# Kernel tuning notes

Hardware: AMD Instinct MI355X
Metric: run time of the kernel (lower is better)

Reference implementation:

```python
import jax, jax.numpy as jnp
import numpy as np

N = 50000      # nodes
E = 1600000    # edges
E_HIDDEN = 256
R_HIDDEN = 128
R = 1000       # number of relations (rel.max()+1)
EPS = 1e-16


def segment_softmax(scores, seg, num_segments):
    # numerically stable softmax over variable-size groups defined by seg
    m = jax.ops.segment_max(scores, seg, num_segments=num_segments)
    ex = jnp.exp(scores - m[seg])
    s = jax.ops.segment_sum(ex, seg, num_segments=num_segments)
    return ex / (s[seg] + EPS)


def setup_inputs() -> dict:
    key = jax.random.key(0)
    ks = jax.random.split(key, 9)
    x_e = jax.random.normal(ks[0], (N, E_HIDDEN), dtype=jnp.float32)
    edge_index = jax.random.randint(ks[1], (2, E), 0, N, dtype=jnp.int64)
    rel = jax.random.randint(ks[2], (E,), 0, R, dtype=jnp.int64)
    # learned params (Linear without bias); stored as [in, out]
    sc_w = 1.0 / np.sqrt(E_HIDDEN)
    sc_a = 1.0 / np.sqrt(R_HIDDEN)
    W_h = jax.random.uniform(ks[3], (E_HIDDEN, R_HIDDEN), jnp.float32, -sc_w, sc_w)
    W_t = jax.random.uniform(ks[4], (E_HIDDEN, R_HIDDEN), jnp.float32, -sc_w, sc_w)
    a_h1 = jax.random.uniform(ks[5], (R_HIDDEN,), jnp.float32, -sc_a, sc_a)
    a_h2 = jax.random.uniform(ks[6], (R_HIDDEN,), jnp.float32, -sc_a, sc_a)
    a_t1 = jax.random.uniform(ks[7], (R_HIDDEN,), jnp.float32, -sc_a, sc_a)
    a_t2 = jax.random.uniform(ks[8], (R_HIDDEN,), jnp.float32, -sc_a, sc_a)
    return {"x_e": x_e, "edge_index": edge_index, "rel": rel,
            "W_h": W_h, "W_t": W_t,
            "a_h1": a_h1, "a_h2": a_h2, "a_t1": a_t1, "a_t2": a_t2}


def reference(x_e, edge_index, rel, W_h, W_t, a_h1, a_h2, a_t1, a_t2):
    h_idx, t_idx = edge_index[0], edge_index[1]
    x_r_h = x_e @ W_h          # [N, r_hidden]
    x_r_t = x_e @ W_t          # [N, r_hidden]
    # per-node scalar scores, gathered per edge
    s_h1 = x_r_h @ a_h1        # [N]
    s_h2 = x_r_t @ a_h2
    s_t1 = x_r_h @ a_t1
    s_t2 = x_r_t @ a_t2
    e1 = s_h1[h_idx] + s_h2[t_idx]   # [E]
    e2 = s_t1[h_idx] + s_t2[t_idx]   # [E]
    alpha1 = segment_softmax(jax.nn.leaky_relu(e1, 0.01), rel, R)
    alpha2 = segment_softmax(jax.nn.leaky_relu(e2, 0.01), rel, R)
    # spmm: out[r] += alpha_e * feat[node_e]
    out_h = jax.ops.segment_sum(alpha1[:, None] * x_r_h[h_idx], rel, num_segments=R)
    out_t = jax.ops.segment_sum(alpha2[:, None] * x_r_t[t_idx], rel, num_segments=R)
    return out_h + out_t       # [R, r_hidden]
```

## Files before the change

### kernel.cpp

```cpp
#include <hip/hip_runtime.h>
#include <hip/hip_fp16.h>
#include <cstdint>
#include <cstddef>

#define E_HID 256
#define R_HID 128
#define NREL  1000
#define EPSF  1e-16f
#define NB    512

__device__ __forceinline__ unsigned encf(float f) {
  unsigned u = __float_as_uint(f);
  return (u & 0x80000000u) ? ~u : (u | 0x80000000u);
}
__device__ __forceinline__ float decf(unsigned u) {
  unsigned b = (u & 0x80000000u) ? (u ^ 0x80000000u) : ~u;
  return __uint_as_float(b);
}

struct h4s { __half2 a, b; };
__device__ __forceinline__ h4s packf4(float4 v) {
  h4s r; r.a = __floats2half2_rn(v.x, v.y); r.b = __floats2half2_rn(v.z, v.w); return r;
}

__global__ __launch_bounds__(256) void k1_gemm(
    const float* __restrict__ xe,
    const float* __restrict__ Wh, const float* __restrict__ Wt,
    const float* __restrict__ ah1, const float* __restrict__ ah2,
    const float* __restrict__ at1, const float* __restrict__ at2,
    __half* __restrict__ xhH, __half* __restrict__ xtH,
    float* __restrict__ sh1, float* __restrict__ sh2,
    float* __restrict__ st1, float* __restrict__ st2, int N)
{
  __shared__ float xT[32][68];
  __shared__ float Wc[32][256];
  const int tid = threadIdx.x;
  const int tx = tid & 15, ty = tid >> 4;
  const int n0 = blockIdx.x * 64;

  float4 acc[4][4];
  #pragma unroll
  for (int n = 0; n < 4; ++n)
    #pragma unroll
    for (int j = 0; j < 4; ++j) acc[n][j] = make_float4(0.f, 0.f, 0.f, 0.f);

  for (int kt = 0; kt < 8; ++kt) {
    const int k0 = kt * 32;
    {
      const int n  = tid >> 2;
      const int kk0 = (tid & 3) * 8;
      float4 v0 = make_float4(0,0,0,0), v1 = make_float4(0,0,0,0);
      if (n0 + n < N) {
        const float* src = xe + (size_t)(n0 + n) * E_HID + k0 + kk0;
        v0 = *(const float4*)(src);
        v1 = *(const float4*)(src + 4);
      }
      xT[kk0+0][n] = v0.x; xT[kk0+1][n] = v0.y; xT[kk0+2][n] = v0.z; xT[kk0+3][n] = v0.w;
      xT[kk0+4][n] = v1.x; xT[kk0+5][n] = v1.y; xT[kk0+6][n] = v1.z; xT[kk0+7][n] = v1.w;
    }
    #pragma unroll
    for (int r2 = 0; r2 < 8; ++r2) {
      const int kk = r2 * 4 + (tid >> 6);
      const int c4 = (tid & 63) * 4;
      float4 wv;
      if (c4 < 128) wv = *(const float4*)(Wh + (size_t)(k0 + kk) * R_HID + c4);
      else          wv = *(const float4*)(Wt + (size_t)(k0 + kk) * R_HID + (c4 - 128));
      *(float4*)&Wc[kk][c4] = wv;
    }
    __syncthreads();
    #pragma unroll 8
    for (int kk = 0; kk < 32; ++kk) {
      const float4 xv = *(const float4*)&xT[kk][ty * 4];
      float4 wv[4];
      wv[0] = *(const float4*)&Wc[kk][      4 * tx];
      wv[1] = *(const float4*)&Wc[kk][ 64 + 4 * tx];
      wv[2] = *(const float4*)&Wc[kk][128 + 4 * tx];
      wv[3] = *(const float4*)&Wc[kk][192 + 4 * tx];
      const float xn[4] = {xv.x, xv.y, xv.z, xv.w};
      #pragma unroll
      for (int n = 0; n < 4; ++n)
        #pragma unroll
        for (int j = 0; j < 4; ++j) {
          acc[n][j].x += xn[n] * wv[j].x;
          acc[n][j].y += xn[n] * wv[j].y;
          acc[n][j].z += xn[n] * wv[j].z;
          acc[n][j].w += xn[n] * wv[j].w;
        }
    }
    __syncthreads();
  }
  float4 vh1[2], vh2[2], vt1[2], vt2[2];
  #pragma unroll
  for (int j = 0; j < 2; ++j) {
    vh1[j] = *(const float4*)(ah1 + 64 * j + 4 * tx);
    vt1[j] = *(const float4*)(at1 + 64 * j + 4 * tx);
    vh2[j] = *(const float4*)(ah2 + 64 * j + 4 * tx);
    vt2[j] = *(const float4*)(at2 + 64 * j + 4 * tx);
  }
  #pragma unroll
  for (int n = 0; n < 4; ++n) {
    const int node = n0 + ty * 4 + n;
    const bool ok = node < N;
    float ph1 = 0.f, ph2 = 0.f, pt1 = 0.f, pt2 = 0.f;
    if (ok) {
      *(h4s*)(xhH + (size_t)node * R_HID +      4 * tx) = packf4(acc[n][0]);
      *(h4s*)(xhH + (size_t)node * R_HID + 64 + 4 * tx) = packf4(acc[n][1]);
      *(h4s*)(xtH + (size_t)node * R_HID +      4 * tx) = packf4(acc[n][2]);
      *(h4s*)(xtH + (size_t)node * R_HID + 64 + 4 * tx) = packf4(acc[n][3]);
      #pragma unroll
      for (int j = 0; j < 2; ++j) {
        ph1 += acc[n][j].x*vh1[j].x + acc[n][j].y*vh1[j].y + acc[n][j].z*vh1[j].z + acc[n][j].w*vh1[j].w;
        pt1 += acc[n][j].x*vt1[j].x + acc[n][j].y*vt1[j].y + acc[n][j].z*vt1[j].z + acc[n][j].w*vt1[j].w;
        ph2 += acc[n][j+2].x*vh2[j].x + acc[n][j+2].y*vh2[j].y + acc[n][j+2].z*vh2[j].z + acc[n][j+2].w*vh2[j].w;
        pt2 += acc[n][j+2].x*vt2[j].x + acc[n][j+2].y*vt2[j].y + acc[n][j+2].z*vt2[j].z + acc[n][j+2].w*vt2[j].w;
      }
    }
    #pragma unroll
    for (int ofs = 1; ofs < 16; ofs <<= 1) {
      ph1 += __shfl_xor(ph1, ofs, 16);
      ph2 += __shfl_xor(ph2, ofs, 16);
      pt1 += __shfl_xor(pt1, ofs, 16);
      pt2 += __shfl_xor(pt2, ofs, 16);
    }
    if (ok && tx == 0) { sh1[node] = ph1; sh2[node] = ph2; st1[node] = pt1; st2[node] = pt2; }
  }
}

__global__ __launch_bounds__(256) void k2_edge(
    const int* __restrict__ ei, const int* __restrict__ rel,
    const float* __restrict__ sh1, const float* __restrict__ sh2,
    const float* __restrict__ st1, const float* __restrict__ st2,
    float* __restrict__ le1, float* __restrict__ le2,
    unsigned* __restrict__ m1u, unsigned* __restrict__ m2u,
    unsigned* __restrict__ blockCnt, int E)
{
  __shared__ unsigned lcnt[NREL];
  __shared__ unsigned lm1[NREL];
  __shared__ unsigned lm2[NREL];
  const int tid = threadIdx.x;
  const unsigned NEG = encf(-1e30f);
  for (int j = tid; j < NREL; j += 256) { lcnt[j] = 0u; lm1[j] = NEG; lm2[j] = NEG; }
  __syncthreads();
  for (int i = blockIdx.x * 256 + tid; i < E; i += NB * 256) {
    int h = ei[i], t = ei[E + i], r = rel[i];
    float e1 = sh1[h] + sh2[t];
    float e2 = st1[h] + st2[t];
    float l1 = e1 >= 0.f ? e1 : 0.01f * e1;
    float l2 = e2 >= 0.f ? e2 : 0.01f * e2;
    le1[i] = l1; le2[i] = l2;
    atomicMax(&lm1[r], encf(l1));
    atomicMax(&lm2[r], encf(l2));
    atomicAdd(&lcnt[r], 1u);
  }
  __syncthreads();
  for (int j = tid; j < NREL; j += 256) {
    blockCnt[(size_t)blockIdx.x * NREL + j] = lcnt[j];
    if (lm1[j] != NEG) atomicMax(m1u + j, lm1[j]);
    if (lm2[j] != NEG) atomicMax(m2u + j, lm2[j]);
  }
}

__global__ __launch_bounds__(64) void k3a_scan(
    const unsigned* __restrict__ blockCnt, unsigned* __restrict__ pre,
    unsigned* __restrict__ cnt)
{
  const int r = blockIdx.x;
  const int lane = threadIdx.x;
  unsigned running = 0u;
  for (int b0 = 0; b0 < NB; b0 += 64) {
    const int b = b0 + lane;
    unsigned v = (b < NB) ? blockCnt[(size_t)b * NREL + r] : 0u;
    unsigned inc = v;
    #pragma unroll
    for (int ofs = 1; ofs < 64; ofs <<= 1) {
      unsigned n = __shfl_up(inc, ofs, 64);
      if (lane >= ofs) inc += n;
    }
    if (b < NB) pre[(size_t)b * NREL + r] = running + inc - v;
    running += __shfl(inc, 63, 64);
  }
  if (lane == 0) cnt[r] = running;
}

__global__ __launch_bounds__(1024) void k3b_scan(
    const unsigned* __restrict__ cnt, unsigned* __restrict__ offs,
    const unsigned* __restrict__ m1u, const unsigned* __restrict__ m2u,
    float* __restrict__ m1f, float* __restrict__ m2f)
{
  __shared__ unsigned s[1024];
  const int t = threadIdx.x;
  s[t] = (t < NREL) ? cnt[t] : 0u;
  __syncthreads();
  for (int ofs = 1; ofs < 1024; ofs <<= 1) {
    unsigned add = (t >= ofs) ? s[t - ofs] : 0u;
    __syncthreads();
    s[t] += add;
    __syncthreads();
  }
  if (t == 0) offs[0] = 0u;
  if (t < NREL) {
    offs[t + 1] = s[t];
    m1f[t] = decf(m1u[t]);
    m2f[t] = decf(m2u[t]);
  }
}

__global__ __launch_bounds__(256) void k4_scatter(
    const int* __restrict__ ei, const int* __restrict__ rel,
    const float* __restrict__ le1, const float* __restrict__ le2,
    const float* __restrict__ m1f, const float* __restrict__ m2f,
    const unsigned* __restrict__ offs, const unsigned* __restrict__ pre,
    float4* __restrict__ meta, int E)
{
  __shared__ unsigned lcur[NREL];
  __shared__ unsigned lbase[NREL];
  __shared__ float lm1[NREL];
  __shared__ float lm2[NREL];
  const int tid = threadIdx.x;
  for (int j = tid; j < NREL; j += 256) {
    lcur[j] = 0u;
    lbase[j] = offs[j] + pre[(size_t)blockIdx.x * NREL + j];
    lm1[j] = m1f[j];
    lm2[j] = m2f[j];
  }
  __syncthreads();
  for (int i = blockIdx.x * 256 + tid; i < E; i += NB * 256) {
    int h = ei[i], t = ei[E + i], r = rel[i];
    float w1 = expf(le1[i] - lm1[r]);
    float w2 = expf(le2[i] - lm2[r]);
    unsigned rank = atomicAdd(&lcur[r], 1u);
    unsigned p = lbase[r] + rank;
    meta[p] = make_float4(__int_as_float(h), __int_as_float(t), w1, w2);
  }
}

#define SPLIT 4
__global__ __launch_bounds__(256) void k5_reduce(
    const unsigned* __restrict__ offs,
    const float4* __restrict__ meta,
    const __half* __restrict__ xhH, const __half* __restrict__ xtH,
    float* __restrict__ accH, float* __restrict__ accT,
    float* __restrict__ S1, float* __restrict__ S2)
{
  const int r    = blockIdx.x >> 2;
  const int sp   = blockIdx.x & 3;
  const int team = threadIdx.x >> 6;
  const int lane = threadIdx.x & 63;
  const unsigned start = offs[r], end = offs[r + 1];
  const unsigned len = end - start;
  const int ci = sp * 4 + team;
  unsigned b0 = start + (unsigned)(((unsigned long long)len * ci) >> 4);
  unsigned b1 = start + (unsigned)(((unsigned long long)len * (ci + 1)) >> 4);
  const int d0 = lane * 2;

  float a1x = 0.f, a1y = 0.f, a2x = 0.f, a2y = 0.f, sw1 = 0.f, sw2 = 0.f;
  unsigned p = b0;
  for (; p + 4 <= b1; p += 4) {
    float4 md[4];
    #pragma unroll
    for (int u = 0; u < 4; ++u) md[u] = meta[p + u];
    #pragma unroll
    for (int u = 0; u < 4; ++u) {
      const int h = __float_as_int(md[u].x);
      const int t = __float_as_int(md[u].y);
      const float w1 = md[u].z, w2 = md[u].w;
      float2 xa = __half22float2(*(const __half2*)(xhH + (size_t)h * R_HID + d0));
      float2 xb = __half22float2(*(const __half2*)(xtH + (size_t)t * R_HID + d0));
      a1x += w1 * xa.x; a1y += w1 * xa.y;
      a2x += w2 * xb.x; a2y += w2 * xb.y;
      sw1 += w1; sw2 += w2;
    }
  }
  for (; p < b1; ++p) {
    float4 md = meta[p];
    const int h = __float_as_int(md.x);
    const int t = __float_as_int(md.y);
    const float w1 = md.z, w2 = md.w;
    float2 xa = __half22float2(*(const __half2*)(xhH + (size_t)h * R_HID + d0));
    float2 xb = __half22float2(*(const __half2*)(xtH + (size_t)t * R_HID + d0));
    a1x += w1 * xa.x; a1y += w1 * xa.y;
    a2x += w2 * xb.x; a2y += w2 * xb.y;
    sw1 += w1; sw2 += w2;
  }
  atomicAdd(accH + (size_t)r * R_HID + d0,     a1x);
  atomicAdd(accH + (size_t)r * R_HID + d0 + 1, a1y);
  atomicAdd(accT + (size_t)r * R_HID + d0,     a2x);
  atomicAdd(accT + (size_t)r * R_HID + d0 + 1, a2y);
  if (lane == 0) { atomicAdd(S1 + r, sw1); atomicAdd(S2 + r, sw2); }
}

__global__ __launch_bounds__(256) void k6_final(
    const float* __restrict__ accH, const float* __restrict__ accT,
    const float* __restrict__ S1, const float* __restrict__ S2,
    float* __restrict__ out)
{
  int i = blockIdx.x * 256 + threadIdx.x;
  if (i >= NREL * R_HID) return;
  int r = i >> 7;
  out[i] = accH[i] / (S1[r] + EPSF) + accT[i] / (S2[r] + EPSF);
}

extern "C" void kernel_launch(void* const* d_in, const int* in_sizes, int n_in,
                              void* d_out, int out_size, void* d_ws, size_t ws_size,
                              hipStream_t stream) {
  const float* xe  = (const float*)d_in[0];
  const int*   ei  = (const int*)d_in[1];
  const int*   rel = (const int*)d_in[2];
  const float* Wh  = (const float*)d_in[3];
  const float* Wt  = (const float*)d_in[4];
  const float* ah1 = (const float*)d_in[5];
  const float* ah2 = (const float*)d_in[6];
  const float* at1 = (const float*)d_in[7];
  const float* at2 = (const float*)d_in[8];
  const int N = in_sizes[0] / E_HID;
  const int E = in_sizes[2];

  char* w = (char*)d_ws;
  size_t o = 0;
  auto alloc = [&](size_t bytes) -> void* {
    void* p = w + o;
    o = (o + bytes + 255) & ~(size_t)255;
    return p;
  };
  __half* xhH = (__half*)alloc((size_t)N * R_HID * 2);
  __half* xtH = (__half*)alloc((size_t)N * R_HID * 2);
  float* sh1 = (float*)alloc((size_t)N * 4);
  float* sh2 = (float*)alloc((size_t)N * 4);
  float* st1 = (float*)alloc((size_t)N * 4);
  float* st2 = (float*)alloc((size_t)N * 4);
  float* le1 = (float*)alloc((size_t)E * 4);
  float* le2 = (float*)alloc((size_t)E * 4);
  float4* meta = (float4*)alloc((size_t)E * 16);
  unsigned* blockCnt = (unsigned*)alloc((size_t)NB * NREL * 4);
  unsigned* pre      = (unsigned*)alloc((size_t)NB * NREL * 4);
  unsigned* cnt      = (unsigned*)alloc((size_t)NREL * 4);
  unsigned* offs     = (unsigned*)alloc((size_t)(NREL + 1) * 4);
  float* m1f = (float*)alloc((size_t)NREL * 4);
  float* m2f = (float*)alloc((size_t)NREL * 4);
  const size_t zstart = o;
  unsigned* m1u = (unsigned*)alloc((size_t)NREL * 4);
  unsigned* m2u = (unsigned*)alloc((size_t)NREL * 4);
  float* S1  = (float*)alloc((size_t)NREL * 4);
  float* S2  = (float*)alloc((size_t)NREL * 4);
  float* accH = (float*)alloc((size_t)NREL * R_HID * 4);
  float* accT = (float*)alloc((size_t)NREL * R_HID * 4);
  const size_t zbytes = o - zstart;

  hipMemsetAsync(w + zstart, 0, zbytes, stream);

  k1_gemm<<<(N + 63) / 64, 256, 0, stream>>>(xe, Wh, Wt, ah1, ah2, at1, at2,
                                             xhH, xtH, sh1, sh2, st1, st2, N);
  k2_edge<<<NB, 256, 0, stream>>>(ei, rel, sh1, sh2, st1, st2,
                                  le1, le2, m1u, m2u, blockCnt, E);
  k3a_scan<<<NREL, 64, 0, stream>>>(blockCnt, pre, cnt);
  k3b_scan<<<1, 1024, 0, stream>>>(cnt, offs, m1u, m2u, m1f, m2f);
  k4_scatter<<<NB, 256, 0, stream>>>(ei, rel, le1, le2, m1f, m2f,
                                     offs, pre, meta, E);
  k5_reduce<<<NREL * SPLIT, 256, 0, stream>>>(offs, meta, xhH, xtH,
                                              accH, accT, S1, S2);
  k6_final<<<(NREL * R_HID + 255) / 256, 256, 0, stream>>>(accH, accT, S1, S2,
                                                           (float*)d_out);
}
```

Before: 322.0 us.

## Use MFMA fp16 GEMM, drop segment max pass, widen reduce loads

```diff
diff --git a/kernel.cpp b/kernel.cpp
--- a/kernel.cpp
+++ b/kernel.cpp
@@ -8,138 +8,212 @@
 #define NREL  1000
 #define EPSF  1e-16f
 #define NB    512
-
-__device__ __forceinline__ unsigned encf(float f) {
-  unsigned u = __float_as_uint(f);
-  return (u & 0x80000000u) ? ~u : (u | 0x80000000u);
-}
-__device__ __forceinline__ float decf(unsigned u) {
-  unsigned b = (u & 0x80000000u) ? (u ^ 0x80000000u) : ~u;
-  return __uint_as_float(b);
-}
-
-struct h4s { __half2 a, b; };
-__device__ __forceinline__ h4s packf4(float4 v) {
-  h4s r; r.a = __floats2half2_rn(v.x, v.y); r.b = __floats2half2_rn(v.z, v.w); return r;
+#define SPLIT 4
+
+typedef _Float16 f16x8 __attribute__((ext_vector_type(8)));
+typedef float f32x4 __attribute__((ext_vector_type(4)));
+
+struct alignas(16) h8 { __half2 a, b, c, d; };
+struct alignas(8)  h4s { __half2 a, b; };
+
+__global__ __launch_bounds__(256) void k0_prep(
+    const float* __restrict__ Wh, const float* __restrict__ Wt,
+    __half* __restrict__ WcT)
+{
+  const int k = blockIdx.x;
+  const int c = threadIdx.x;
+  const float v = (c < R_HID) ? Wh[(size_t)k * R_HID + c]
+                              : Wt[(size_t)k * R_HID + (c - R_HID)];
+  WcT[(size_t)c * E_HID + k] = __float2half(v);
 }
 
 __global__ __launch_bounds__(256) void k1_gemm(
-    const float* __restrict__ xe,
-    const float* __restrict__ Wh, const float* __restrict__ Wt,
+    const float* __restrict__ xe, const __half* __restrict__ WcT,
     const float* __restrict__ ah1, const float* __restrict__ ah2,
     const float* __restrict__ at1, const float* __restrict__ at2,
     __half* __restrict__ xhH, __half* __restrict__ xtH,
     float* __restrict__ sh1, float* __restrict__ sh2,
     float* __restrict__ st1, float* __restrict__ st2, int N)
 {
-  __shared__ float xT[32][68];
-  __shared__ float Wc[32][256];
-  const int tid = threadIdx.x;
-  const int tx = tid & 15, ty = tid >> 4;
-  const int n0 = blockIdx.x * 64;
-
-  float4 acc[4][4];
-  #pragma unroll
-  for (int n = 0; n < 4; ++n)
-    #pragma unroll
-    for (int j = 0; j < 4; ++j) acc[n][j] = make_float4(0.f, 0.f, 0.f, 0.f);
+  __shared__ __half As[128 * 32];
+  __shared__ __half Bs[128 * 32];
+  __shared__ float sA[2][128];
+  __shared__ float sB[2][128];
+
+  const int tid  = threadIdx.x;
+  const int lane = tid & 63;
+  const int wid  = tid >> 6;
+  const int wr = wid >> 1, wc = wid & 1;
+  const int nbm = (N + 127) >> 7;
+  const int mb = blockIdx.x % nbm;
+  const int cb = blockIdx.x / nbm;
+  const int n0 = mb * 128;
+
+  f32x4 acc[4][4];
+  #pragma unroll
+  for (int m = 0; m < 4; ++m)
+    #pragma unroll
+    for (int n = 0; n < 4; ++n) acc[m][n] = (f32x4){0.f, 0.f, 0.f, 0.f};
+
+  const int arow = tid >> 1, ah = tid & 1;
+  const bool aok = (n0 + arow) < N;
+  const float*  xsrc = xe + (size_t)(n0 + arow) * E_HID + ah * 16;
+  const __half* bsrc = WcT + ((size_t)(cb * 128 + arow) << 8) + ah * 16;
+  __half* Aw = &As[arow * 32 + ah * 16];
+  __half* Bw = &Bs[arow * 32 + ah * 16];
+
+  const int fr = lane & 15, fq = lane >> 4;
 
   for (int kt = 0; kt < 8; ++kt) {
-    const int k0 = kt * 32;
-    {
-      const int n  = tid >> 2;
-      const int kk0 = (tid & 3) * 8;
-      float4 v0 = make_float4(0,0,0,0), v1 = make_float4(0,0,0,0);
-      if (n0 + n < N) {
-        const float* src = xe + (size_t)(n0 + n) * E_HID + k0 + kk0;
-        v0 = *(const float4*)(src);
-        v1 = *(const float4*)(src + 4);
-      }
-      xT[kk0+0][n] = v0.x; xT[kk0+1][n] = v0.y; xT[kk0+2][n] = v0.z; xT[kk0+3][n] = v0.w;
-      xT[kk0+4][n] = v1.x; xT[kk0+5][n] = v1.y; xT[kk0+6][n] = v1.z; xT[kk0+7][n] = v1.w;
-    }
-    #pragma unroll
-    for (int r2 = 0; r2 < 8; ++r2) {
-      const int kk = r2 * 4 + (tid >> 6);
-      const int c4 = (tid & 63) * 4;
-      float4 wv;
-      if (c4 < 128) wv = *(const float4*)(Wh + (size_t)(k0 + kk) * R_HID + c4);
-      else          wv = *(const float4*)(Wt + (size_t)(k0 + kk) * R_HID + (c4 - 128));
-      *(float4*)&Wc[kk][c4] = wv;
-    }
     __syncthreads();
-    #pragma unroll 8
-    for (int kk = 0; kk < 32; ++kk) {
-      const float4 xv = *(const float4*)&xT[kk][ty * 4];
-      float4 wv[4];
-      wv[0] = *(const float4*)&Wc[kk][      4 * tx];
-      wv[1] = *(const float4*)&Wc[kk][ 64 + 4 * tx];
-      wv[2] = *(const float4*)&Wc[kk][128 + 4 * tx];
-      wv[3] = *(const float4*)&Wc[kk][192 + 4 * tx];
-      const float xn[4] = {xv.x, xv.y, xv.z, xv.w};
+    float4 v0 = make_float4(0,0,0,0), v1 = v0, v2 = v0, v3 = v0;
+    if (aok) {
+      const float* s = xsrc + kt * 32;
+      v0 = *(const float4*)(s);     v1 = *(const float4*)(s + 4);
+      v2 = *(const float4*)(s + 8); v3 = *(const float4*)(s + 12);
+    }
+    h8 p0, p1;
+    p0.a = __floats2half2_rn(v0.x, v0.y); p0.b = __floats2half2_rn(v0.z, v0.w);
+    p0.c = __floats2half2_rn(v1.x, v1.y); p0.d = __floats2half2_rn(v1.z, v1.w);
+    p1.a = __floats2half2_rn(v2.x, v2.y); p1.b = __floats2half2_rn(v2.z, v2.w);
+    p1.c = __floats2half2_rn(v3.x, v3.y); p1.d = __floats2half2_rn(v3.z, v3.w);
+    *(h8*)(Aw) = p0; *(h8*)(Aw + 8) = p1;
+    float4 b0 = *(const float4*)(bsrc + kt * 32);
+    float4 b1 = *(const float4*)(bsrc + kt * 32 + 8);
+    *(float4*)(Bw) = b0; *(float4*)(Bw + 8) = b1;
+    __syncthreads();
+    f16x8 aF[4], bF[4];
+    #pragma unroll
+    for (int m = 0; m < 4; ++m)
+      aF[m] = *(const f16x8*)&As[(wr * 64 + m * 16 + fr) * 32 + fq * 8];
+    #pragma unroll
+    for (int n = 0; n < 4; ++n)
+      bF[n] = *(const f16x8*)&Bs[(wc * 64 + n * 16 + fr) * 32 + fq * 8];
+    #pragma unroll
+    for (int m = 0; m < 4; ++m)
       #pragma unroll
       for (int n = 0; n < 4; ++n)
+        acc[m][n] = __builtin_amdgcn_mfma_f32_16x16x32_f16(aF[m], bF[n], acc[m][n], 0, 0, 0);
+  }
+
+  __half* dst = (cb == 0) ? xhH : xtH;
+  #pragma unroll
+  for (int m = 0; m < 4; ++m) {
+    const int rl0 = wr * 64 + m * 16 + fq * 4;
+    #pragma unroll
+    for (int r = 0; r < 4; ++r) {
+      const int node = n0 + rl0 + r;
+      if (node < N) {
         #pragma unroll
-        for (int j = 0; j < 4; ++j) {
-          acc[n][j].x += xn[n] * wv[j].x;
-          acc[n][j].y += xn[n] * wv[j].y;
-          acc[n][j].z += xn[n] * wv[j].z;
-          acc[n][j].w += xn[n] * wv[j].w;
-        }
-    }
+        for (int n = 0; n < 4; ++n)
+          dst[(size_t)node * R_HID + wc * 64 + n * 16 + fr] = __float2half(acc[m][n][r]);
+      }
+    }
+  }
+
+  const float* aV1 = (cb == 0) ? ah1 : ah2;
+  const float* aV2 = (cb == 0) ? at1 : at2;
+  float avA[4], avB[4];
+  #pragma unroll
+  for (int n = 0; n < 4; ++n) {
+    avA[n] = aV1[wc * 64 + n * 16 + fr];
+    avB[n] = aV2[wc * 64 + n * 16 + fr];
+  }
+  #pragma unroll
+  for (int m = 0; m < 4; ++m)
+    #pragma unroll
+    for (int r = 0; r < 4; ++r) {
+      float vA = acc[m][0][r]*avA[0] + acc[m][1][r]*avA[1]
+               + acc[m][2][r]*avA[2] + acc[m][3][r]*avA[3];
+      float vB = acc[m][0][r]*avB[0] + acc[m][1][r]*avB[1]
+               + acc[m][2][r]*avB[2] + acc[m][3][r]*avB[3];
+      #pragma unroll
+      for (int ofs = 1; ofs < 16; ofs <<= 1) {
+        vA += __shfl_xor(vA, ofs, 16);
+        vB += __shfl_xor(vB, ofs, 16);
+      }
+      if (fr == 0) {
+        const int rl = wr * 64 + m * 16 + fq * 4 + r;
+        sA[wc][rl] = vA;
+        sB[wc][rl] = vB;
+      }
+    }
+  __syncthreads();
+  if (tid < 128 && n0 + tid < N) {
+    float* o1 = (cb == 0) ? sh1 : sh2;
+    float* o2 = (cb == 0) ? st1 : st2;
+    o1[n0 + tid] = sA[0][tid] + sA[1][tid];
+    o2[n0 + tid] = sB[0][tid] + sB[1][tid];
+  }
+}
+
+__global__ __launch_bounds__(256) void k2_hist(
+    const int* __restrict__ rel, unsigned* __restrict__ blockCnt, int E)
+{
+  __shared__ unsigned lcnt[NREL];
+  const int tid = threadIdx.x;
+  for (int j = tid; j < NREL; j += 256) lcnt[j] = 0u;
+  __syncthreads();
+  for (int i = blockIdx.x * 256 + tid; i < E; i += NB * 256)
+    atomicAdd(&lcnt[rel[i]], 1u);
+  __syncthreads();
+  for (int j = tid; j < NREL; j += 256)
+    blockCnt[(size_t)blockIdx.x * NREL + j] = lcnt[j];
+}
+
+__global__ __launch_bounds__(64) void k3a_scan(
+    const unsigned* __restrict__ blockCnt, unsigned* __restrict__ pre,
+    unsigned* __restrict__ cnt)
+{
+  const int r = blockIdx.x;
+  const int lane = threadIdx.x;
+  unsigned running = 0u;
+  for (int b0 = 0; b0 < NB; b0 += 64) {
+    const int b = b0 + lane;
+    unsigned v = blockCnt[(size_t)b * NREL + r];
+    unsigned inc = v;
+    #pragma unroll
+    for (int ofs = 1; ofs < 64; ofs <<= 1) {
+      unsigned nv = __shfl_up(inc, ofs, 64);
+      if (lane >= ofs) inc += nv;
+    }
+    pre[(size_t)b * NREL + r] = running + inc - v;
+    running += __shfl(inc, 63, 64);
+  }
+  if (lane == 0) cnt[r] = running;
+}
+
+__global__ __launch_bounds__(1024) void k3b_scan(
+    const unsigned* __restrict__ cnt, unsigned* __restrict__ offs)
+{
+  __shared__ unsigned s[1024];
+  const int t = threadIdx.x;
+  s[t] = (t < NREL) ? cnt[t] : 0u;
+  __syncthreads();
+  for (int ofs = 1; ofs < 1024; ofs <<= 1) {
+    unsigned add = (t >= ofs) ? s[t - ofs] : 0u;
     __syncthreads();
-  }
-  float4 vh1[2], vh2[2], vt1[2], vt2[2];
-  #pragma unroll
-  for (int j = 0; j < 2; ++j) {
-    vh1[j] = *(const float4*)(ah1 + 64 * j + 4 * tx);
-    vt1[j] = *(const float4*)(at1 + 64 * j + 4 * tx);
-    vh2[j] = *(const float4*)(ah2 + 64 * j + 4 * tx);
-    vt2[j] = *(const float4*)(at2 + 64 * j + 4 * tx);
-  }
-  #pragma unroll
-  for (int n = 0; n < 4; ++n) {
-    const int node = n0 + ty * 4 + n;
-    const bool ok = node < N;
-    float ph1 = 0.f, ph2 = 0.f, pt1 = 0.f, pt2 = 0.f;
-    if (ok) {
-      *(h4s*)(xhH + (size_t)node * R_HID +      4 * tx) = packf4(acc[n][0]);
-      *(h4s*)(xhH + (size_t)node * R_HID + 64 + 4 * tx) = packf4(acc[n][1]);
-      *(h4s*)(xtH + (size_t)node * R_HID +      4 * tx) = packf4(acc[n][2]);
-      *(h4s*)(xtH + (size_t)node * R_HID + 64 + 4 * tx) = packf4(acc[n][3]);
-      #pragma unroll
-      for (int j = 0; j < 2; ++j) {
-        ph1 += acc[n][j].x*vh1[j].x + acc[n][j].y*vh1[j].y + acc[n][j].z*vh1[j].z + acc[n][j].w*vh1[j].w;
-        pt1 += acc[n][j].x*vt1[j].x + acc[n][j].y*vt1[j].y + acc[n][j].z*vt1[j].z + acc[n][j].w*vt1[j].w;
-        ph2 += acc[n][j+2].x*vh2[j].x + acc[n][j+2].y*vh2[j].y + acc[n][j+2].z*vh2[j].z + acc[n][j+2].w*vh2[j].w;
-        pt2 += acc[n][j+2].x*vt2[j].x + acc[n][j+2].y*vt2[j].y + acc[n][j+2].z*vt2[j].z + acc[n][j+2].w*vt2[j].w;
-      }
-    }
-    #pragma unroll
-    for (int ofs = 1; ofs < 16; ofs <<= 1) {
-      ph1 += __shfl_xor(ph1, ofs, 16);
-      ph2 += __shfl_xor(ph2, ofs, 16);
-      pt1 += __shfl_xor(pt1, ofs, 16);
-      pt2 += __shfl_xor(pt2, ofs, 16);
-    }
-    if (ok && tx == 0) { sh1[node] = ph1; sh2[node] = ph2; st1[node] = pt1; st2[node] = pt2; }
-  }
-}
-
-__global__ __launch_bounds__(256) void k2_edge(
+    s[t] += add;
+    __syncthreads();
+  }
+  if (t == 0) offs[0] = 0u;
+  if (t < NREL) offs[t + 1] = s[t];
+}
+
+__global__ __launch_bounds__(256) void k4_scatter(
     const int* __restrict__ ei, const int* __restrict__ rel,
     const float* __restrict__ sh1, const float* __restrict__ sh2,
     const float* __restrict__ st1, const float* __restrict__ st2,
-    float* __restrict__ le1, float* __restrict__ le2,
-    unsigned* __restrict__ m1u, unsigned* __restrict__ m2u,
-    unsigned* __restrict__ blockCnt, int E)
-{
-  __shared__ unsigned lcnt[NREL];
-  __shared__ unsigned lm1[NREL];
-  __shared__ unsigned lm2[NREL];
+    const unsigned* __restrict__ offs, const unsigned* __restrict__ pre,
+    float4* __restrict__ meta, int E)
+{
+  __shared__ unsigned lcur[NREL];
+  __shared__ unsigned lbase[NREL];
   const int tid = threadIdx.x;
-  const unsigned NEG = encf(-1e30f);
-  for (int j = tid; j < NREL; j += 256) { lcnt[j] = 0u; lm1[j] = NEG; lm2[j] = NEG; }
+  for (int j = tid; j < NREL; j += 256) {
+    lcur[j] = 0u;
+    lbase[j] = offs[j] + pre[(size_t)blockIdx.x * NREL + j];
+  }
   __syncthreads();
   for (int i = blockIdx.x * 256 + tid; i < E; i += NB * 256) {
     int h = ei[i], t = ei[E + i], r = rel[i];
@@ -147,94 +221,14 @@
     float e2 = st1[h] + st2[t];
     float l1 = e1 >= 0.f ? e1 : 0.01f * e1;
     float l2 = e2 >= 0.f ? e2 : 0.01f * e2;
-    le1[i] = l1; le2[i] = l2;
-    atomicMax(&lm1[r], encf(l1));
-    atomicMax(&lm2[r], encf(l2));
-    atomicAdd(&lcnt[r], 1u);
-  }
-  __syncthreads();
-  for (int j = tid; j < NREL; j += 256) {
-    blockCnt[(size_t)blockIdx.x * NREL + j] = lcnt[j];
-    if (lm1[j] != NEG) atomicMax(m1u + j, lm1[j]);
-    if (lm2[j] != NEG) atomicMax(m2u + j, lm2[j]);
-  }
-}
-
-__global__ __launch_bounds__(64) void k3a_scan(
-    const unsigned* __restrict__ blockCnt, unsigned* __restrict__ pre,
-    unsigned* __restrict__ cnt)
-{
-  const int r = blockIdx.x;
-  const int lane = threadIdx.x;
-  unsigned running = 0u;
-  for (int b0 = 0; b0 < NB; b0 += 64) {
-    const int b = b0 + lane;
-    unsigned v = (b < NB) ? blockCnt[(size_t)b * NREL + r] : 0u;
-    unsigned inc = v;
-    #pragma unroll
-    for (int ofs = 1; ofs < 64; ofs <<= 1) {
-      unsigned n = __shfl_up(inc, ofs, 64);
-      if (lane >= ofs) inc += n;
-    }
-    if (b < NB) pre[(size_t)b * NREL + r] = running + inc - v;
-    running += __shfl(inc, 63, 64);
-  }
-  if (lane == 0) cnt[r] = running;
-}
-
-__global__ __launch_bounds__(1024) void k3b_scan(
-    const unsigned* __restrict__ cnt, unsigned* __restrict__ offs,
-    const unsigned* __restrict__ m1u, const unsigned* __restrict__ m2u,
-    float* __restrict__ m1f, float* __restrict__ m2f)
-{
-  __shared__ unsigned s[1024];
-  const int t = threadIdx.x;
-  s[t] = (t < NREL) ? cnt[t] : 0u;
-  __syncthreads();
-  for (int ofs = 1; ofs < 1024; ofs <<= 1) {
-    unsigned add = (t >= ofs) ? s[t - ofs] : 0u;
-    __syncthreads();
-    s[t] += add;
-    __syncthreads();
-  }
-  if (t == 0) offs[0] = 0u;
-  if (t < NREL) {
-    offs[t + 1] = s[t];
-    m1f[t] = decf(m1u[t]);
-    m2f[t] = decf(m2u[t]);
-  }
-}
-
-__global__ __launch_bounds__(256) void k4_scatter(
-    const int* __restrict__ ei, const int* __restrict__ rel,
-    const float* __restrict__ le1, const float* __restrict__ le2,
-    const float* __restrict__ m1f, const float* __restrict__ m2f,
-    const unsigned* __restrict__ offs, const unsigned* __restrict__ pre,
-    float4* __restrict__ meta, int E)
-{
-  __shared__ unsigned lcur[NREL];
-  __shared__ unsigned lbase[NREL];
-  __shared__ float lm1[NREL];
-  __shared__ float lm2[NREL];
-  const int tid = threadIdx.x;
-  for (int j = tid; j < NREL; j += 256) {
-    lcur[j] = 0u;
-    lbase[j] = offs[j] + pre[(size_t)blockIdx.x * NREL + j];
-    lm1[j] = m1f[j];
-    lm2[j] = m2f[j];
-  }
-  __syncthreads();
-  for (int i = blockIdx.x * 256 + tid; i < E; i += NB * 256) {
-    int h = ei[i], t = ei[E + i], r = rel[i];
-    float w1 = expf(le1[i] - lm1[r]);
-    float w2 = expf(le2[i] - lm2[r]);
+    float w1 = expf(l1);
+    float w2 = expf(l2);
     unsigned rank = atomicAdd(&lcur[r], 1u);
     unsigned p = lbase[r] + rank;
     meta[p] = make_float4(__int_as_float(h), __int_as_float(t), w1, w2);
   }
 }
 
-#define SPLIT 4
 __global__ __launch_bounds__(256) void k5_reduce(
     const unsigned* __restrict__ offs,
     const float4* __restrict__ meta,
@@ -246,47 +240,55 @@
   const int sp   = blockIdx.x & 3;
   const int team = threadIdx.x >> 6;
   const int lane = threadIdx.x & 63;
+  const int es   = lane >> 5;
+  const int dl   = lane & 31;
+  const int d0   = dl * 4;
   const unsigned start = offs[r], end = offs[r + 1];
   const unsigned len = end - start;
   const int ci = sp * 4 + team;
-  unsigned b0 = start + (unsigned)(((unsigned long long)len * ci) >> 4);
-  unsigned b1 = start + (unsigned)(((unsigned long long)len * (ci + 1)) >> 4);
-  const int d0 = lane * 2;
-
-  float a1x = 0.f, a1y = 0.f, a2x = 0.f, a2y = 0.f, sw1 = 0.f, sw2 = 0.f;
-  unsigned p = b0;
-  for (; p + 4 <= b1; p += 4) {
-    float4 md[4];
-    #pragma unroll
-    for (int u = 0; u < 4; ++u) md[u] = meta[p + u];
+  const unsigned b0 = start + (unsigned)(((unsigned long long)len * ci) >> 4);
+  const unsigned b1 = start + (unsigned)(((unsigned long long)len * (ci + 1)) >> 4);
+
+  float a1[4] = {0.f, 0.f, 0.f, 0.f};
+  float a2[4] = {0.f, 0.f, 0.f, 0.f};
+  float sw1 = 0.f, sw2 = 0.f;
+
+  for (unsigned base = b0; base < b1; base += 8) {
     #pragma unroll
     for (int u = 0; u < 4; ++u) {
-      const int h = __float_as_int(md[u].x);
-      const int t = __float_as_int(md[u].y);
-      const float w1 = md[u].z, w2 = md[u].w;
-      float2 xa = __half22float2(*(const __half2*)(xhH + (size_t)h * R_HID + d0));
-      float2 xb = __half22float2(*(const __half2*)(xtH + (size_t)t * R_HID + d0));
-      a1x += w1 * xa.x; a1y += w1 * xa.y;
-      a2x += w2 * xb.x; a2y += w2 * xb.y;
-      sw1 += w1; sw2 += w2;
-    }
-  }
-  for (; p < b1; ++p) {
-    float4 md = meta[p];
-    const int h = __float_as_int(md.x);
-    const int t = __float_as_int(md.y);
-    const float w1 = md.z, w2 = md.w;
-    float2 xa = __half22float2(*(const __half2*)(xhH + (size_t)h * R_HID + d0));
-    float2 xb = __half22float2(*(const __half2*)(xtH + (size_t)t * R_HID + d0));
-    a1x += w1 * xa.x; a1y += w1 * xa.y;
-    a2x += w2 * xb.x; a2y += w2 * xb.y;
-    sw1 += w1; sw2 += w2;
-  }
-  atomicAdd(accH + (size_t)r * R_HID + d0,     a1x);
-  atomicAdd(accH + (size_t)r * R_HID + d0 + 1, a1y);
-  atomicAdd(accT + (size_t)r * R_HID + d0,     a2x);
-  atomicAdd(accT + (size_t)r * R_HID + d0 + 1, a2y);
-  if (lane == 0) { atomicAdd(S1 + r, sw1); atomicAdd(S2 + r, sw2); }
+      const unsigned idx = base + 2u * u + (unsigned)es;
+      if (idx < b1) {
+        const float4 md = meta[idx];
+        const int h = __float_as_int(md.x);
+        const int t = __float_as_int(md.y);
+        const float w1 = md.z, w2 = md.w;
+        h4s va = *(const h4s*)(xhH + (size_t)h * R_HID + d0);
+        h4s vb = *(const h4s*)(xtH + (size_t)t * R_HID + d0);
+        float2 fa0 = __half22float2(va.a), fa1 = __half22float2(va.b);
+        float2 fb0 = __half22float2(vb.a), fb1 = __half22float2(vb.b);
+        a1[0] += w1 * fa0.x; a1[1] += w1 * fa0.y;
+        a1[2] += w1 * fa1.x; a1[3] += w1 * fa1.y;
+        a2[0] += w2 * fb0.x; a2[1] += w2 * fb0.y;
+        a2[2] += w2 * fb1.x; a2[3] += w2 * fb1.y;
+        sw1 += w1; sw2 += w2;
+      }
+    }
+  }
+  #pragma unroll
+  for (int j = 0; j < 4; ++j) {
+    a1[j] += __shfl_xor(a1[j], 32);
+    a2[j] += __shfl_xor(a2[j], 32);
+  }
+  sw1 += __shfl_xor(sw1, 32);
+  sw2 += __shfl_xor(sw2, 32);
+  if (lane < 32) {
+    #pragma unroll
+    for (int j = 0; j < 4; ++j) {
+      atomicAdd(accH + (size_t)r * R_HID + d0 + j, a1[j]);
+      atomicAdd(accT + (size_t)r * R_HID + d0 + j, a2[j]);
+    }
+    if (lane == 0) { atomicAdd(S1 + r, sw1); atomicAdd(S2 + r, sw2); }
+  }
 }
 
 __global__ __launch_bounds__(256) void k6_final(
@@ -322,24 +324,19 @@
     o = (o + bytes + 255) & ~(size_t)255;
     return p;
   };
+  __half* WcT = (__half*)alloc((size_t)E_HID * E_HID * 2);
   __half* xhH = (__half*)alloc((size_t)N * R_HID * 2);
   __half* xtH = (__half*)alloc((size_t)N * R_HID * 2);
   float* sh1 = (float*)alloc((size_t)N * 4);
   float* sh2 = (float*)alloc((size_t)N * 4);
   float* st1 = (float*)alloc((size_t)N * 4);
   float* st2 = (float*)alloc((size_t)N * 4);
-  float* le1 = (float*)alloc((size_t)E * 4);
-  float* le2 = (float*)alloc((size_t)E * 4);
   float4* meta = (float4*)alloc((size_t)E * 16);
   unsigned* blockCnt = (unsigned*)alloc((size_t)NB * NREL * 4);
   unsigned* pre      = (unsigned*)alloc((size_t)NB * NREL * 4);
   unsigned* cnt      = (unsigned*)alloc((size_t)NREL * 4);
   unsigned* offs     = (unsigned*)alloc((size_t)(NREL + 1) * 4);
-  float* m1f = (float*)alloc((size_t)NREL * 4);
-  float* m2f = (float*)alloc((size_t)NREL * 4);
   const size_t zstart = o;
-  unsigned* m1u = (unsigned*)alloc((size_t)NREL * 4);
-  unsigned* m2u = (unsigned*)alloc((size_t)NREL * 4);
   float* S1  = (float*)alloc((size_t)NREL * 4);
   float* S2  = (float*)alloc((size_t)NREL * 4);
   float* accH = (float*)alloc((size_t)NREL * R_HID * 4);
@@ -348,13 +345,14 @@
 
   hipMemsetAsync(w + zstart, 0, zbytes, stream);
 
-  k1_gemm<<<(N + 63) / 64, 256, 0, stream>>>(xe, Wh, Wt, ah1, ah2, at1, at2,
-                                             xhH, xtH, sh1, sh2, st1, st2, N);
-  k2_edge<<<NB, 256, 0, stream>>>(ei, rel, sh1, sh2, st1, st2,
-                                  le1, le2, m1u, m2u, blockCnt, E);
+  const int nbm = (N + 127) >> 7;
+  k0_prep<<<E_HID, 256, 0, stream>>>(Wh, Wt, WcT);
+  k1_gemm<<<nbm * 2, 256, 0, stream>>>(xe, WcT, ah1, ah2, at1, at2,
+                                       xhH, xtH, sh1, sh2, st1, st2, N);
+  k2_hist<<<NB, 256, 0, stream>>>(rel, blockCnt, E);
   k3a_scan<<<NREL, 64, 0, stream>>>(blockCnt, pre, cnt);
-  k3b_scan<<<1, 1024, 0, stream>>>(cnt, offs, m1u, m2u, m1f, m2f);
-  k4_scatter<<<NB, 256, 0, stream>>>(ei, rel, le1, le2, m1f, m2f,
+  k3b_scan<<<1, 1024, 0, stream>>>(cnt, offs);
+  k4_scatter<<<NB, 256, 0, stream>>>(ei, rel, sh1, sh2, st1, st2,
                                      offs, pre, meta, E);
   k5_reduce<<<NREL * SPLIT, 256, 0, stream>>>(offs, meta, xhH, xtH,
                                               accH, accT, S1, S2);
```

After: 264.2 us. -18.0%, faster.
